# Kernel optimization log

Hardware: AMD Instinct MI355X
Metric: run time of the kernel (lower is better)

Reference implementation:

```python
import jax, jax.numpy as jnp
import numpy as np

B, S, D = 16, 1024, 768
H = 12
DH = D // H  # 64

def setup_inputs() -> dict:
    key = jax.random.key(0)
    ks = jax.random.split(key, 7)
    scale = 1.0 / np.sqrt(D)
    return {
        "hidden_states": jax.random.normal(ks[0], (B, S, D), dtype=jnp.float32),
        "Wq": jax.random.normal(ks[1], (D, D), dtype=jnp.float32) * scale,
        "bq": jnp.zeros((D,), dtype=jnp.float32),
        "Wk": jax.random.normal(ks[2], (D, D), dtype=jnp.float32) * scale,
        "bk": jnp.zeros((D,), dtype=jnp.float32),
        "Wv": jax.random.normal(ks[3], (D, D), dtype=jnp.float32) * scale,
        "bv": jnp.zeros((D,), dtype=jnp.float32),
    }

def reference(hidden_states, Wq, bq, Wk, bk, Wv, bv):
    # QKV projections: [B,S,D] -> [B,S,H,DH] -> [B,H,S,DH]
    def proj(W, b):
        y = hidden_states @ W.T + b
        return y.reshape(B, S, H, DH).transpose(0, 2, 1, 3)
    q = proj(Wq, bq)
    k = proj(Wk, bk)
    v = proj(Wv, bv)
    # attention scores [B,H,S,S], scaled by sqrt(d_head)
    scores = jnp.einsum('bhqd,bhkd->bhqk', q, k) / jnp.sqrt(jnp.float32(DH))
    probs = jax.nn.softmax(scores, axis=-1)
    # dropout prob = 0.0 (eval) -> identity
    ctx = jnp.einsum('bhqk,bhkd->bhqd', probs, v)
    ctx = ctx.transpose(0, 2, 1, 3).reshape(B, S, D)
    return ctx
```

## Files before the change

kernel.cpp:

```cpp
#include <hip/hip_runtime.h>
#include <hip/hip_bf16.h>

typedef __attribute__((ext_vector_type(8))) short short8;
typedef __attribute__((ext_vector_type(4))) float float4v;
typedef __attribute__((ext_vector_type(2))) unsigned int uint2v;

#define MFMA_BF16 __builtin_amdgcn_mfma_f32_16x16x32_bf16

__device__ __forceinline__ unsigned short f2b(float f) {
  union { float f; unsigned u; } v; v.f = f;
  unsigned r = v.u + 0x7FFFu + ((v.u >> 16) & 1u);
  return (unsigned short)(r >> 16);
}

__device__ __forceinline__ unsigned pk2(float x, float y) {
  float2 v; v.x = x; v.y = y;
  __hip_bfloat162 h = __float22bfloat162_rn(v);
  union { __hip_bfloat162 h; unsigned u; } c; c.h = h;
  return c.u;
}

__device__ __forceinline__ void gld16(const unsigned short* g, unsigned short* l) {
  __builtin_amdgcn_global_load_lds(
      (const __attribute__((address_space(1))) unsigned int*)g,
      (__attribute__((address_space(3))) unsigned int*)l, 16, 0, 0);
}

__device__ __forceinline__ int swa(int r, int k) {
  return (r << 6) + ((((k >> 3) ^ r ^ (r >> 3)) & 7) << 3) + (k & 7);
}

__global__ __launch_bounds__(256) void cast_all(
    const float* __restrict__ hs, const float* __restrict__ Wq,
    const float* __restrict__ Wk, const float* __restrict__ Wv,
    unsigned short* __restrict__ Xb, unsigned short* __restrict__ Wb) {
  const int blk = blockIdx.x;
  const float* src;
  unsigned short* dst;
  int i;
  if (blk < 12288) {
    i = blk * 256 + threadIdx.x;
    src = hs;
    dst = Xb;
  } else {
    const int x = blk - 12288;
    const int z = x / 576;
    i = (x - z * 576) * 256 + threadIdx.x;
    src = (z == 0) ? Wq : (z == 1 ? Wk : Wv);
    dst = Wb + (size_t)z * 589824;
  }
  float4 f = ((const float4*)src)[i];
  uint2 o;
  o.x = pk2(f.x, f.y);
  o.y = pk2(f.z, f.w);
  ((uint2*)dst)[i] = o;
}

__global__ __launch_bounds__(512) void qkv_gemm(
    const unsigned short* __restrict__ X, const unsigned short* __restrict__ Wall,
    const float* __restrict__ b0, const float* __restrict__ b1, const float* __restrict__ b2,
    unsigned short* __restrict__ O0, unsigned short* __restrict__ O1, unsigned short* __restrict__ OVT) {
  extern __shared__ __align__(16) unsigned short LDS[];

  const int g = blockIdx.x;
  const int orig = (g & 7) * 144 + (g >> 3);
  const int mblk = orig / 18;
  const int nblk = orig - mblk * 18;
  const int m0 = mblk * 256, n0p = nblk * 128;

  const int t = threadIdx.x, w = t >> 6, l = t & 63, qd = l >> 4, col = l & 15;
  const int wm64 = (w & 3) * 64, wn64 = (w >> 2) * 64;
  const int qd8 = qd * 8;

  const int cA0 = t, cA1 = 512 + t, cA2 = 1024 + t, cA3 = 1536 + t;
  const int rA0 = cA0 >> 3, rA1 = cA1 >> 3, rA2 = cA2 >> 3, rA3 = cA3 >> 3;
  const int pA0 = (cA0 ^ rA0 ^ (rA0 >> 3)) & 7, pA1 = (cA1 ^ rA1 ^ (rA1 >> 3)) & 7;
  const int pA2 = (cA2 ^ rA2 ^ (rA2 >> 3)) & 7, pA3 = (cA3 ^ rA3 ^ (rA3 >> 3)) & 7;
  const int cB0 = t, cB1 = 512 + t;
  const int rB0 = cB0 >> 3, rB1 = cB1 >> 3;
  const int pB0 = (cB0 ^ rB0 ^ (rB0 >> 3)) & 7, pB1 = (cB1 ^ rB1 ^ (rB1 >> 3)) & 7;

  const unsigned short* Xa0 = X + (size_t)(m0 + rA0) * 768 + pA0 * 8;
  const unsigned short* Xa1 = X + (size_t)(m0 + rA1) * 768 + pA1 * 8;
  const unsigned short* Xa2 = X + (size_t)(m0 + rA2) * 768 + pA2 * 8;
  const unsigned short* Xa3 = X + (size_t)(m0 + rA3) * 768 + pA3 * 8;
  const unsigned short* Wb0 = Wall + (size_t)(n0p + rB0) * 768 + pB0 * 8;
  const unsigned short* Wb1 = Wall + (size_t)(n0p + rB1) * 768 + pB1 * 8;
  const int dA0 = cA0 * 8, dA1 = cA1 * 8, dA2 = cA2 * 8, dA3 = cA3 * 8;
  const int dB0 = cB0 * 8, dB1 = cB1 * 8;

#define STAGE(kt, sb)                                         \
  do {                                                        \
    unsigned short* SA_ = LDS + (sb)*24576;                   \
    unsigned short* SB_ = SA_ + 16384;                        \
    const int kk_ = (kt)*64;                                  \
    gld16(Xa0 + kk_, SA_ + dA0);                              \
    gld16(Xa1 + kk_, SA_ + dA1);                              \
    gld16(Xa2 + kk_, SA_ + dA2);                              \
    gld16(Xa3 + kk_, SA_ + dA3);                              \
    gld16(Wb0 + kk_, SB_ + dB0);                              \
    gld16(Wb1 + kk_, SB_ + dB1);                              \
  } while (0)

  float4v acc[4][4];
#pragma unroll
  for (int i = 0; i < 4; ++i)
#pragma unroll
    for (int j = 0; j < 4; ++j) acc[i][j] = (float4v)0.0f;

#define COMPUTE(cur)                                                          \
  do {                                                                        \
    const unsigned short* Ar_ = LDS + (cur)*24576;                            \
    const unsigned short* Br_ = Ar_ + 16384;                                  \
    _Pragma("unroll") for (int ks = 0; ks < 2; ++ks) {                        \
      short8 af[4], bf[4];                                                    \
      _Pragma("unroll") for (int mi = 0; mi < 4; ++mi)                        \
          af[mi] = *(const short8*)&Ar_[swa(wm64 + mi * 16 + col,             \
                                            ks * 32 + qd8)];                  \
      _Pragma("unroll") for (int ni = 0; ni < 4; ++ni)                        \
          bf[ni] = *(const short8*)&Br_[swa(wn64 + ni * 16 + col,             \
                                            ks * 32 + qd8)];                  \
      __builtin_amdgcn_s_setprio(1);                                          \
      _Pragma("unroll") for (int mi = 0; mi < 4; ++mi)                        \
          _Pragma("unroll") for (int ni = 0; ni < 4; ++ni)                    \
          acc[mi][ni] = MFMA_BF16(af[mi], bf[ni], acc[mi][ni], 0, 0, 0);      \
      __builtin_amdgcn_s_setprio(0);                                          \
    }                                                                         \
  } while (0)

  STAGE(0, 0);
  STAGE(1, 1);
  asm volatile("s_waitcnt vmcnt(6)" ::: "memory");
  __builtin_amdgcn_s_barrier();
  __builtin_amdgcn_sched_barrier(0);

  int cur = 0;
#pragma unroll 1
  for (int kt = 0; kt < 10; ++kt) {
    const int sb = (cur == 0) ? 2 : cur - 1;
    STAGE(kt + 2, sb);
    COMPUTE(cur);
    asm volatile("s_waitcnt vmcnt(6)" ::: "memory");
    __builtin_amdgcn_s_barrier();
    __builtin_amdgcn_sched_barrier(0);
    cur = (cur == 2) ? 0 : cur + 1;
  }
  COMPUTE(cur);
  asm volatile("s_waitcnt vmcnt(0)" ::: "memory");
  __builtin_amdgcn_s_barrier();
  __builtin_amdgcn_sched_barrier(0);
  cur = (cur == 2) ? 0 : cur + 1;
  COMPUTE(cur);

  const int zz = n0p / 768;
  const int nbase = n0p - zz * 768;

  if (zz < 2) {
    unsigned short* O = (zz == 0) ? O0 : O1;
    const float* bias = (zz == 0) ? b0 : b1;
    const float osc = (zz == 0) ? 0.18033688f : 1.0f;
#pragma unroll
    for (int ni = 0; ni < 4; ++ni) {
      const int n = nbase + wn64 + ni * 16 + col;
      const float bb = bias[n];
#pragma unroll
      for (int mi = 0; mi < 4; ++mi)
#pragma unroll
        for (int r = 0; r < 4; ++r) {
          const int m = m0 + wm64 + mi * 16 + qd * 4 + r;
          O[(size_t)m * 768 + n] = f2b((acc[mi][ni][r] + bb) * osc);
        }
    }
  } else {
    __syncthreads();
    unsigned short* T = LDS;
#pragma unroll
    for (int ni = 0; ni < 4; ++ni) {
      const int nl = wn64 + ni * 16 + col;
      const float bb = b2[nbase + nl];
#pragma unroll
      for (int mi = 0; mi < 4; ++mi) {
        const int ml = wm64 + mi * 16 + qd * 4;
        const int mc = ml >> 3;
        ushort4 o;
        o.x = f2b(acc[mi][ni][0] + bb);
        o.y = f2b(acc[mi][ni][1] + bb);
        o.z = f2b(acc[mi][ni][2] + bb);
        o.w = f2b(acc[mi][ni][3] + bb);
        *(ushort4*)&T[(nl << 8) + (((mc ^ (nl & 31)) & 31) << 3) + (ml & 7)] = o;
      }
    }
    __syncthreads();
    const int nl2 = t >> 2;
    const int seg = t & 3;
    const int nglob = nbase + nl2;
    const int hh = nglob >> 6, dd = nglob & 63;
    const int bb2 = m0 >> 10;
    unsigned short* dstp =
        &OVT[(((size_t)bb2 * 12 + hh) * 64 + dd) * 1024 + (m0 & 1023) + seg * 64];
#pragma unroll
    for (int j = 0; j < 8; ++j) {
      const int mc = seg * 8 + j;
      uint4 vv = *(const uint4*)&T[(nl2 << 8) + (((mc ^ (nl2 & 31)) & 31) << 3)];
      *(uint4*)&dstp[j * 8] = vv;
    }
  }
#undef STAGE
#undef COMPUTE
}

__global__ __launch_bounds__(256) void attn(
    const unsigned short* __restrict__ Q, const unsigned short* __restrict__ K,
    const unsigned short* __restrict__ VT, float* __restrict__ O) {
  __shared__ __align__(16) unsigned short Ks0[4096];
  __shared__ __align__(16) unsigned short Ks1[4096];
  __shared__ __align__(16) unsigned short Vt0[4096];
  __shared__ __align__(16) unsigned short Vt1[4096];

  const int g = blockIdx.x;
  const int orig = (g & 7) * 192 + (g >> 3);
  const int qt = orig & 7;
  const int hb = orig >> 3;
  const int b = hb / 12;
  const int h = hb - b * 12;

  const int t = threadIdx.x, w = t >> 6, l = t & 63, qd = l >> 4, col = l & 15;
  const size_t bh = (size_t)b * 786432 + (size_t)h * 64;
  const unsigned short* Kb = K + bh;
  const unsigned short* VTb = VT + ((size_t)(b * 12 + h)) * 65536;

  short8 qf[2][2];
  {
    const unsigned short* Qg = Q + bh + (size_t)(qt * 128 + w * 32) * 768;
#pragma unroll
    for (int mi = 0; mi < 2; ++mi)
#pragma unroll
      for (int ks = 0; ks < 2; ++ks)
        qf[mi][ks] =
            *(const short8*)&Qg[(size_t)(mi * 16 + col) * 768 + ks * 32 + qd * 8];
  }

  const int c0 = t, c1 = 256 + t;
  const int r0 = c0 >> 3, cc0 = (c0 ^ r0 ^ (r0 >> 3)) & 7;
  const int r1 = c1 >> 3, cc1 = (c1 ^ r1 ^ (r1 >> 3)) & 7;

#define STAGE_K(ktile, dst)                                             \
  do {                                                                  \
    const unsigned short* Kg_ = Kb + (size_t)(ktile)*49152;             \
    gld16(&Kg_[(size_t)r0 * 768 + cc0 * 8], &dst[c0 * 8]);              \
    gld16(&Kg_[(size_t)r1 * 768 + cc1 * 8], &dst[c1 * 8]);              \
  } while (0)

#define STAGE_V(ktile, dst)                                             \
  do {                                                                  \
    const unsigned short* Vg_ = VTb + (ktile)*64;                       \
    gld16(&Vg_[(size_t)r0 * 1024 + cc0 * 8], &dst[c0 * 8]);             \
    gld16(&Vg_[(size_t)r1 * 1024 + cc1 * 8], &dst[c1 * 8]);             \
  } while (0)

  STAGE_K(0, Ks0);
  STAGE_V(0, Vt0);

  float4v acc[2][4];
  float4v accl[2];
#pragma unroll
  for (int mi = 0; mi < 2; ++mi) {
    accl[mi] = (float4v)0.0f;
#pragma unroll
    for (int dt = 0; dt < 4; ++dt) acc[mi][dt] = (float4v)0.0f;
  }

  short8 ones;
#pragma unroll
  for (int j = 0; j < 8; ++j) ones[j] = (short)0x3F80;

  __syncthreads();

#define ATTN_ITER(kt, KsR, VtR, KsW, VtW)                                 \
  do {                                                                    \
    if ((kt) < 15) {                                                      \
      STAGE_K((kt) + 1, KsW);                                             \
      STAGE_V((kt) + 1, VtW);                                             \
    }                                                                     \
    short8 kf[2][4];                                                      \
    _Pragma("unroll") for (int ks = 0; ks < 2; ++ks)                      \
        _Pragma("unroll") for (int ni = 0; ni < 4; ++ni)                  \
        kf[ks][ni] =                                                      \
        *(const short8*)&KsR[swa(ni * 16 + col, ks * 32 + qd * 8)];       \
    float4v sT[2][4];                                                     \
    _Pragma("unroll") for (int mi = 0; mi < 2; ++mi)                      \
        _Pragma("unroll") for (int ni = 0; ni < 4; ++ni)                  \
        sT[mi][ni] = (float4v)0.0f;                                       \
    __builtin_amdgcn_s_setprio(1);                                        \
    _Pragma("unroll") for (int ks = 0; ks < 2; ++ks)                      \
        _Pragma("unroll") for (int ni = 0; ni < 4; ++ni) {                \
      sT[0][ni] = MFMA_BF16(kf[ks][ni], qf[0][ks], sT[0][ni], 0, 0, 0);   \
      sT[1][ni] = MFMA_BF16(kf[ks][ni], qf[1][ks], sT[1][ni], 0, 0, 0);   \
    }                                                                     \
    __builtin_amdgcn_s_setprio(0);                                        \
    _Pragma("unroll") for (int s = 0; s < 2; ++s) {                       \
      short8 pf[2];                                                       \
      _Pragma("unroll") for (int mi = 0; mi < 2; ++mi) {                  \
        float4v sa = sT[mi][s * 2 + 0];                                   \
        float4v sb = sT[mi][s * 2 + 1];                                   \
        unsigned A0 = pk2(__builtin_amdgcn_exp2f(sa[0]),                  \
                          __builtin_amdgcn_exp2f(sa[1]));                 \
        unsigned A1 = pk2(__builtin_amdgcn_exp2f(sa[2]),                  \
                          __builtin_amdgcn_exp2f(sa[3]));                 \
        unsigned B0 = pk2(__builtin_amdgcn_exp2f(sb[0]),                  \
                          __builtin_amdgcn_exp2f(sb[1]));                 \
        unsigned B1 = pk2(__builtin_amdgcn_exp2f(sb[2]),                  \
                          __builtin_amdgcn_exp2f(sb[3]));                 \
        uint2v x0 = __builtin_amdgcn_permlane32_swap(A0, B0, false, false);   \
        uint2v x1 = __builtin_amdgcn_permlane32_swap(A1, B1, false, false);   \
        uint2v y02 = __builtin_amdgcn_permlane16_swap(x0[0], x0[1], false, false); \
        uint2v y13 = __builtin_amdgcn_permlane16_swap(x1[0], x1[1], false, false); \
        union { unsigned u[4]; short8 v; } pu;                            \
        pu.u[0] = y02[0]; pu.u[1] = y13[0];                               \
        pu.u[2] = y02[1]; pu.u[3] = y13[1];                               \
        pf[mi] = pu.v;                                                    \
      }                                                                   \
      const int kk = s * 32 + qd * 8;                                     \
      __builtin_amdgcn_s_setprio(1);                                      \
      _Pragma("unroll") for (int dt = 0; dt < 4; ++dt) {                  \
        short8 vf = *(const short8*)&VtR[swa(dt * 16 + col, kk)];         \
        acc[0][dt] = MFMA_BF16(vf, pf[0], acc[0][dt], 0, 0, 0);           \
        acc[1][dt] = MFMA_BF16(vf, pf[1], acc[1][dt], 0, 0, 0);           \
      }                                                                   \
      accl[0] = MFMA_BF16(ones, pf[0], accl[0], 0, 0, 0);                 \
      accl[1] = MFMA_BF16(ones, pf[1], accl[1], 0, 0, 0);                 \
      __builtin_amdgcn_s_setprio(0);                                      \
    }                                                                     \
    __syncthreads();                                                      \
  } while (0)

  for (int kt2 = 0; kt2 < 16; kt2 += 2) {
    ATTN_ITER(kt2, Ks0, Vt0, Ks1, Vt1);
    ATTN_ITER(kt2 + 1, Ks1, Vt1, Ks0, Vt0);
  }

  float* Og = O + (size_t)(b * 1024 + qt * 128) * 768 + h * 64;
#pragma unroll
  for (int mi = 0; mi < 2; ++mi) {
    const float rl = 1.0f / accl[mi][0];
    const int q = w * 32 + mi * 16 + col;
#pragma unroll
    for (int dt = 0; dt < 4; ++dt) {
      float4 o;
      o.x = acc[mi][dt][0] * rl;
      o.y = acc[mi][dt][1] * rl;
      o.z = acc[mi][dt][2] * rl;
      o.w = acc[mi][dt][3] * rl;
      *(float4*)&Og[(size_t)q * 768 + dt * 16 + qd * 4] = o;
    }
  }
#undef STAGE_K
#undef STAGE_V
#undef ATTN_ITER
}

extern "C" void kernel_launch(void* const* d_in, const int* in_sizes, int n_in,
                              void* d_out, int out_size, void* d_ws, size_t ws_size,
                              hipStream_t stream) {
  const float* hs = (const float*)d_in[0];
  const float* Wq = (const float*)d_in[1];
  const float* bq = (const float*)d_in[2];
  const float* Wk = (const float*)d_in[3];
  const float* bk = (const float*)d_in[4];
  const float* Wv = (const float*)d_in[5];
  const float* bv = (const float*)d_in[6];
  float* out = (float*)d_out;
  char* ws = (char*)d_ws;

  unsigned short* Xb = (unsigned short*)ws;
  unsigned short* Wb = (unsigned short*)(ws + 25165824);
  unsigned short* Qb = (unsigned short*)(ws + 28704768);
  unsigned short* Kb = (unsigned short*)(ws + 53870592);
  unsigned short* Vb = (unsigned short*)(ws + 79036416);

  static bool attr_set = false;
  if (!attr_set) {
    hipFuncSetAttribute((const void*)qkv_gemm,
                        hipFuncAttributeMaxDynamicSharedMemorySize, 147456);
    attr_set = true;
  }

  cast_all<<<14016, 256, 0, stream>>>(hs, Wq, Wk, Wv, Xb, Wb);

  qkv_gemm<<<dim3(1152), 512, 147456, stream>>>(Xb, Wb, bq, bk, bv, Qb, Kb, Vb);

  attn<<<dim3(1536), 256, 0, stream>>>(Qb, Kb, Vb, out);
}
```

Measured before the change: 258.6 us.

## Fuse fp32-to-bf16 cast into QKV GEMM loads, drop separate cast kernel

Removes the standalone cast kernel. The QKV GEMM now reads fp32 activations and weights from global memory into registers, converts them to bf16, and writes them to swizzled LDS. The pipeline changes from a 3-stage direct global-to-LDS async copy to a 2-stage register-staged double buffer with __syncthreads. This saves one kernel launch and the bf16 round trip through memory, but the GEMM now reads twice as many bytes per tile (fp32), and each weight is converted many times across blocks. It also loses the deeper async pipeline.

New measurement: 320.7 us. +24.0%, slower.

```diff
diff --git a/kernel.cpp b/kernel.cpp
--- a/kernel.cpp
+++ b/kernel.cpp
@@ -30,34 +30,9 @@
   return (r << 6) + ((((k >> 3) ^ r ^ (r >> 3)) & 7) << 3) + (k & 7);
 }
 
-__global__ __launch_bounds__(256) void cast_all(
-    const float* __restrict__ hs, const float* __restrict__ Wq,
-    const float* __restrict__ Wk, const float* __restrict__ Wv,
-    unsigned short* __restrict__ Xb, unsigned short* __restrict__ Wb) {
-  const int blk = blockIdx.x;
-  const float* src;
-  unsigned short* dst;
-  int i;
-  if (blk < 12288) {
-    i = blk * 256 + threadIdx.x;
-    src = hs;
-    dst = Xb;
-  } else {
-    const int x = blk - 12288;
-    const int z = x / 576;
-    i = (x - z * 576) * 256 + threadIdx.x;
-    src = (z == 0) ? Wq : (z == 1 ? Wk : Wv);
-    dst = Wb + (size_t)z * 589824;
-  }
-  float4 f = ((const float4*)src)[i];
-  uint2 o;
-  o.x = pk2(f.x, f.y);
-  o.y = pk2(f.z, f.w);
-  ((uint2*)dst)[i] = o;
-}
-
 __global__ __launch_bounds__(512) void qkv_gemm(
-    const unsigned short* __restrict__ X, const unsigned short* __restrict__ Wall,
+    const float* __restrict__ Xf, const float* __restrict__ Wqf,
+    const float* __restrict__ Wkf, const float* __restrict__ Wvf,
     const float* __restrict__ b0, const float* __restrict__ b1, const float* __restrict__ b2,
     unsigned short* __restrict__ O0, unsigned short* __restrict__ O1, unsigned short* __restrict__ OVT) {
   extern __shared__ __align__(16) unsigned short LDS[];
@@ -67,46 +42,68 @@
   const int mblk = orig / 18;
   const int nblk = orig - mblk * 18;
   const int m0 = mblk * 256, n0p = nblk * 128;
+  const int zz = n0p / 768;
+  const int nbase = n0p - zz * 768;
+  const float* Wf = (zz == 0) ? Wqf : (zz == 1 ? Wkf : Wvf);
 
   const int t = threadIdx.x, w = t >> 6, l = t & 63, qd = l >> 4, col = l & 15;
   const int wm64 = (w & 3) * 64, wn64 = (w >> 2) * 64;
   const int qd8 = qd * 8;
 
-  const int cA0 = t, cA1 = 512 + t, cA2 = 1024 + t, cA3 = 1536 + t;
-  const int rA0 = cA0 >> 3, rA1 = cA1 >> 3, rA2 = cA2 >> 3, rA3 = cA3 >> 3;
-  const int pA0 = (cA0 ^ rA0 ^ (rA0 >> 3)) & 7, pA1 = (cA1 ^ rA1 ^ (rA1 >> 3)) & 7;
-  const int pA2 = (cA2 ^ rA2 ^ (rA2 >> 3)) & 7, pA3 = (cA3 ^ rA3 ^ (rA3 >> 3)) & 7;
-  const int cB0 = t, cB1 = 512 + t;
-  const int rB0 = cB0 >> 3, rB1 = cB1 >> 3;
-  const int pB0 = (cB0 ^ rB0 ^ (rB0 >> 3)) & 7, pB1 = (cB1 ^ rB1 ^ (rB1 >> 3)) & 7;
-
-  const unsigned short* Xa0 = X + (size_t)(m0 + rA0) * 768 + pA0 * 8;
-  const unsigned short* Xa1 = X + (size_t)(m0 + rA1) * 768 + pA1 * 8;
-  const unsigned short* Xa2 = X + (size_t)(m0 + rA2) * 768 + pA2 * 8;
-  const unsigned short* Xa3 = X + (size_t)(m0 + rA3) * 768 + pA3 * 8;
-  const unsigned short* Wb0 = Wall + (size_t)(n0p + rB0) * 768 + pB0 * 8;
-  const unsigned short* Wb1 = Wall + (size_t)(n0p + rB1) * 768 + pB1 * 8;
-  const int dA0 = cA0 * 8, dA1 = cA1 * 8, dA2 = cA2 * 8, dA3 = cA3 * 8;
-  const int dB0 = cB0 * 8, dB1 = cB1 * 8;
-
-#define STAGE(kt, sb)                                         \
-  do {                                                        \
-    unsigned short* SA_ = LDS + (sb)*24576;                   \
-    unsigned short* SB_ = SA_ + 16384;                        \
-    const int kk_ = (kt)*64;                                  \
-    gld16(Xa0 + kk_, SA_ + dA0);                              \
-    gld16(Xa1 + kk_, SA_ + dA1);                              \
-    gld16(Xa2 + kk_, SA_ + dA2);                              \
-    gld16(Xa3 + kk_, SA_ + dA3);                              \
-    gld16(Wb0 + kk_, SB_ + dB0);                              \
-    gld16(Wb1 + kk_, SB_ + dB1);                              \
+  const int j = t & 7, tr = t >> 3;
+  const int rA0 = tr, rA1 = 64 + tr, rA2 = 128 + tr, rA3 = 192 + tr;
+  const int rB0 = tr, rB1 = 64 + tr;
+  const int dA0 = (rA0 << 6) + (((j ^ rA0 ^ (rA0 >> 3)) & 7) << 3);
+  const int dA1 = (rA1 << 6) + (((j ^ rA1 ^ (rA1 >> 3)) & 7) << 3);
+  const int dA2 = (rA2 << 6) + (((j ^ rA2 ^ (rA2 >> 3)) & 7) << 3);
+  const int dA3 = (rA3 << 6) + (((j ^ rA3 ^ (rA3 >> 3)) & 7) << 3);
+  const int dB0 = (rB0 << 6) + (((j ^ rB0 ^ (rB0 >> 3)) & 7) << 3);
+  const int dB1 = (rB1 << 6) + (((j ^ rB1 ^ (rB1 >> 3)) & 7) << 3);
+  const float* XA0 = Xf + (size_t)(m0 + rA0) * 768 + j * 8;
+  const float* XA1 = Xf + (size_t)(m0 + rA1) * 768 + j * 8;
+  const float* XA2 = Xf + (size_t)(m0 + rA2) * 768 + j * 8;
+  const float* XA3 = Xf + (size_t)(m0 + rA3) * 768 + j * 8;
+  const float* WB0 = Wf + (size_t)(nbase + rB0) * 768 + j * 8;
+  const float* WB1 = Wf + (size_t)(nbase + rB1) * 768 + j * 8;
+
+  float4 a0, a1, a2, a3, a4, a5, a6, a7, g0, g1, g2, g3;
+
+#define LOADR(kt)                                              \
+  do {                                                         \
+    const int kk_ = (kt)*64;                                   \
+    a0 = *(const float4*)(XA0 + kk_); a1 = *(const float4*)(XA0 + kk_ + 4); \
+    a2 = *(const float4*)(XA1 + kk_); a3 = *(const float4*)(XA1 + kk_ + 4); \
+    a4 = *(const float4*)(XA2 + kk_); a5 = *(const float4*)(XA2 + kk_ + 4); \
+    a6 = *(const float4*)(XA3 + kk_); a7 = *(const float4*)(XA3 + kk_ + 4); \
+    g0 = *(const float4*)(WB0 + kk_); g1 = *(const float4*)(WB0 + kk_ + 4); \
+    g2 = *(const float4*)(WB1 + kk_); g3 = *(const float4*)(WB1 + kk_ + 4); \
+  } while (0)
+
+#define CVW(base, dst, lo, hi)                                 \
+  do {                                                         \
+    uint4 pv_;                                                 \
+    pv_.x = pk2(lo.x, lo.y); pv_.y = pk2(lo.z, lo.w);          \
+    pv_.z = pk2(hi.x, hi.y); pv_.w = pk2(hi.z, hi.w);          \
+    *(uint4*)&base[dst] = pv_;                                 \
+  } while (0)
+
+#define WRITEALL(sb)                                           \
+  do {                                                         \
+    unsigned short* SA_ = LDS + (sb)*24576;                    \
+    unsigned short* SB_ = SA_ + 16384;                         \
+    CVW(SA_, dA0, a0, a1);                                     \
+    CVW(SA_, dA1, a2, a3);                                     \
+    CVW(SA_, dA2, a4, a5);                                     \
+    CVW(SA_, dA3, a6, a7);                                     \
+    CVW(SB_, dB0, g0, g1);                                     \
+    CVW(SB_, dB1, g2, g3);                                     \
   } while (0)
 
   float4v acc[4][4];
 #pragma unroll
   for (int i = 0; i < 4; ++i)
 #pragma unroll
-    for (int j = 0; j < 4; ++j) acc[i][j] = (float4v)0.0f;
+    for (int jj = 0; jj < 4; ++jj) acc[i][jj] = (float4v)0.0f;
 
 #define COMPUTE(cur)                                                          \
   do {                                                                        \
@@ -128,32 +125,21 @@
     }                                                                         \
   } while (0)
 
-  STAGE(0, 0);
-  STAGE(1, 1);
-  asm volatile("s_waitcnt vmcnt(6)" ::: "memory");
-  __builtin_amdgcn_s_barrier();
-  __builtin_amdgcn_sched_barrier(0);
+  LOADR(0);
+  WRITEALL(0);
+  __syncthreads();
 
   int cur = 0;
 #pragma unroll 1
-  for (int kt = 0; kt < 10; ++kt) {
-    const int sb = (cur == 0) ? 2 : cur - 1;
-    STAGE(kt + 2, sb);
+  for (int kt = 0; kt < 11; ++kt) {
+    LOADR(kt + 1);
+    __builtin_amdgcn_sched_barrier(0);
     COMPUTE(cur);
-    asm volatile("s_waitcnt vmcnt(6)" ::: "memory");
-    __builtin_amdgcn_s_barrier();
-    __builtin_amdgcn_sched_barrier(0);
-    cur = (cur == 2) ? 0 : cur + 1;
+    WRITEALL(cur ^ 1);
+    __syncthreads();
+    cur ^= 1;
   }
   COMPUTE(cur);
-  asm volatile("s_waitcnt vmcnt(0)" ::: "memory");
-  __builtin_amdgcn_s_barrier();
-  __builtin_amdgcn_sched_barrier(0);
-  cur = (cur == 2) ? 0 : cur + 1;
-  COMPUTE(cur);
-
-  const int zz = n0p / 768;
-  const int nbase = n0p - zz * 768;
 
   if (zz < 2) {
     unsigned short* O = (zz == 0) ? O0 : O1;
@@ -199,13 +185,15 @@
     unsigned short* dstp =
         &OVT[(((size_t)bb2 * 12 + hh) * 64 + dd) * 1024 + (m0 & 1023) + seg * 64];
 #pragma unroll
-    for (int j = 0; j < 8; ++j) {
-      const int mc = seg * 8 + j;
+    for (int jj = 0; jj < 8; ++jj) {
+      const int mc = seg * 8 + jj;
       uint4 vv = *(const uint4*)&T[(nl2 << 8) + (((mc ^ (nl2 & 31)) & 31) << 3)];
-      *(uint4*)&dstp[j * 8] = vv;
+      *(uint4*)&dstp[jj * 8] = vv;
     }
   }
-#undef STAGE
+#undef LOADR
+#undef CVW
+#undef WRITEALL
 #undef COMPUTE
 }
 
@@ -272,7 +260,7 @@
 
   short8 ones;
 #pragma unroll
-  for (int j = 0; j < 8; ++j) ones[j] = (short)0x3F80;
+  for (int jj = 0; jj < 8; ++jj) ones[jj] = (short)0x3F80;
 
   __syncthreads();
 
@@ -372,22 +360,19 @@
   float* out = (float*)d_out;
   char* ws = (char*)d_ws;
 
-  unsigned short* Xb = (unsigned short*)ws;
-  unsigned short* Wb = (unsigned short*)(ws + 25165824);
-  unsigned short* Qb = (unsigned short*)(ws + 28704768);
-  unsigned short* Kb = (unsigned short*)(ws + 53870592);
-  unsigned short* Vb = (unsigned short*)(ws + 79036416);
+  unsigned short* Qb = (unsigned short*)ws;
+  unsigned short* Kb = (unsigned short*)(ws + 25165824);
+  unsigned short* Vb = (unsigned short*)(ws + 50331648);
 
   static bool attr_set = false;
   if (!attr_set) {
     hipFuncSetAttribute((const void*)qkv_gemm,
-                        hipFuncAttributeMaxDynamicSharedMemorySize, 147456);
+                        hipFuncAttributeMaxDynamicSharedMemorySize, 98304);
     attr_set = true;
   }
 
-  cast_all<<<14016, 256, 0, stream>>>(hs, Wq, Wk, Wv, Xb, Wb);
-
-  qkv_gemm<<<dim3(1152), 512, 147456, stream>>>(Xb, Wb, bq, bk, bv, Qb, Kb, Vb);
+  qkv_gemm<<<dim3(1152), 512, 98304, stream>>>(hs, Wq, Wk, Wv, bq, bk, bv,
+                                               Qb, Kb, Vb);
 
   attn<<<dim3(1536), 256, 0, stream>>>(Qb, Kb, Vb, out);
 }
```

## Software-pipeline attention loop with triple-buffered K/V and QK one tile ahead

Applied to the files above, without the earlier changes.

Restructures the attention inner loop so the QK^T MFMAs for tile kt run in the same step as the exp/softmax and PV work for tile kt-1. K is prefetched two tiles ahead and V one tile ahead through a third LDS buffer. Full __syncthreads is replaced by explicit vmcnt waits plus raw barriers. The goal is to hide exp/permlane latency and global-to-LDS load latency behind matrix work. In exchange it uses more LDS (48KB instead of 32KB) and keeps two score sets live in registers, which may reduce occupancy.

New measurement: 253.8 us. About the same (-1.9%).

```diff
diff --git a/kernel.cpp b/kernel.cpp
--- a/kernel.cpp
+++ b/kernel.cpp
@@ -214,8 +214,10 @@
     const unsigned short* __restrict__ VT, float* __restrict__ O) {
   __shared__ __align__(16) unsigned short Ks0[4096];
   __shared__ __align__(16) unsigned short Ks1[4096];
+  __shared__ __align__(16) unsigned short Ks2[4096];
   __shared__ __align__(16) unsigned short Vt0[4096];
   __shared__ __align__(16) unsigned short Vt1[4096];
+  __shared__ __align__(16) unsigned short Vt2[4096];
 
   const int g = blockIdx.x;
   const int orig = (g & 7) * 192 + (g >> 3);
@@ -258,9 +260,6 @@
     gld16(&Vg_[(size_t)r1 * 1024 + cc1 * 8], &dst[c1 * 8]);             \
   } while (0)
 
-  STAGE_K(0, Ks0);
-  STAGE_V(0, Vt0);
-
   float4v acc[2][4];
   float4v accl[2];
 #pragma unroll
@@ -269,40 +268,39 @@
 #pragma unroll
     for (int dt = 0; dt < 4; ++dt) acc[mi][dt] = (float4v)0.0f;
   }
+  float4v sA[2][4], sB[2][4];
+  const float4v Zv = (float4v)0.0f;
 
   short8 ones;
 #pragma unroll
   for (int j = 0; j < 8; ++j) ones[j] = (short)0x3F80;
 
-  __syncthreads();
-
-#define ATTN_ITER(kt, KsR, VtR, KsW, VtW)                                 \
+#define QK_TILE(KsR, S)                                                   \
   do {                                                                    \
-    if ((kt) < 15) {                                                      \
-      STAGE_K((kt) + 1, KsW);                                             \
-      STAGE_V((kt) + 1, VtW);                                             \
-    }                                                                     \
     short8 kf[2][4];                                                      \
     _Pragma("unroll") for (int ks = 0; ks < 2; ++ks)                      \
         _Pragma("unroll") for (int ni = 0; ni < 4; ++ni)                  \
         kf[ks][ni] =                                                      \
         *(const short8*)&KsR[swa(ni * 16 + col, ks * 32 + qd * 8)];       \
-    float4v sT[2][4];                                                     \
-    _Pragma("unroll") for (int mi = 0; mi < 2; ++mi)                      \
-        _Pragma("unroll") for (int ni = 0; ni < 4; ++ni)                  \
-        sT[mi][ni] = (float4v)0.0f;                                       \
     __builtin_amdgcn_s_setprio(1);                                        \
-    _Pragma("unroll") for (int ks = 0; ks < 2; ++ks)                      \
-        _Pragma("unroll") for (int ni = 0; ni < 4; ++ni) {                \
-      sT[0][ni] = MFMA_BF16(kf[ks][ni], qf[0][ks], sT[0][ni], 0, 0, 0);   \
-      sT[1][ni] = MFMA_BF16(kf[ks][ni], qf[1][ks], sT[1][ni], 0, 0, 0);   \
+    _Pragma("unroll") for (int ni = 0; ni < 4; ++ni) {                    \
+      S[0][ni] = MFMA_BF16(kf[0][ni], qf[0][0], Zv, 0, 0, 0);             \
+      S[1][ni] = MFMA_BF16(kf[0][ni], qf[1][0], Zv, 0, 0, 0);             \
+    }                                                                     \
+    _Pragma("unroll") for (int ni = 0; ni < 4; ++ni) {                    \
+      S[0][ni] = MFMA_BF16(kf[1][ni], qf[0][1], S[0][ni], 0, 0, 0);       \
+      S[1][ni] = MFMA_BF16(kf[1][ni], qf[1][1], S[1][ni], 0, 0, 0);       \
     }                                                                     \
     __builtin_amdgcn_s_setprio(0);                                        \
+  } while (0)
+
+#define SMPV(S, VtR)                                                      \
+  do {                                                                    \
     _Pragma("unroll") for (int s = 0; s < 2; ++s) {                       \
       short8 pf[2];                                                       \
       _Pragma("unroll") for (int mi = 0; mi < 2; ++mi) {                  \
-        float4v sa = sT[mi][s * 2 + 0];                                   \
-        float4v sb = sT[mi][s * 2 + 1];                                   \
+        float4v sa = S[mi][s * 2 + 0];                                    \
+        float4v sb = S[mi][s * 2 + 1];                                    \
         unsigned A0 = pk2(__builtin_amdgcn_exp2f(sa[0]),                  \
                           __builtin_amdgcn_exp2f(sa[1]));                 \
         unsigned A1 = pk2(__builtin_amdgcn_exp2f(sa[2]),                  \
@@ -331,13 +329,54 @@
       accl[1] = MFMA_BF16(ones, pf[1], accl[1], 0, 0, 0);                 \
       __builtin_amdgcn_s_setprio(0);                                      \
     }                                                                     \
-    __syncthreads();                                                      \
-  } while (0)
-
-  for (int kt2 = 0; kt2 < 16; kt2 += 2) {
-    ATTN_ITER(kt2, Ks0, Vt0, Ks1, Vt1);
-    ATTN_ITER(kt2 + 1, Ks1, Vt1, Ks0, Vt0);
-  }
+  } while (0)
+
+#define W4 asm volatile("s_waitcnt vmcnt(4)" ::: "memory")
+#define W2 asm volatile("s_waitcnt vmcnt(2)" ::: "memory")
+#define W0 asm volatile("s_waitcnt vmcnt(0)" ::: "memory")
+#define BAR                                                               \
+  do {                                                                    \
+    __builtin_amdgcn_s_barrier();                                         \
+    __builtin_amdgcn_sched_barrier(0);                                    \
+  } while (0)
+
+#define PIPE(kt, KR, VR, KW, VW, Snew, Sold, WAIT)                        \
+  do {                                                                    \
+    if ((kt) + 2 < 16) STAGE_K((kt) + 2, KW);                             \
+    if ((kt) + 1 < 16) STAGE_V((kt) + 1, VW);                             \
+    QK_TILE(KR, Snew);                                                    \
+    SMPV(Sold, VR);                                                       \
+    WAIT;                                                                 \
+    BAR;                                                                  \
+  } while (0)
+
+  STAGE_K(0, Ks0);
+  STAGE_V(0, Vt0);
+  STAGE_K(1, Ks1);
+  STAGE_V(1, Vt1);
+  STAGE_K(2, Ks2);
+  W0;
+  BAR;
+  QK_TILE(Ks0, sA);
+  BAR;
+
+  PIPE(1,  Ks1, Vt0, Ks0, Vt2, sB, sA, W4);
+  PIPE(2,  Ks2, Vt1, Ks1, Vt0, sA, sB, W4);
+  PIPE(3,  Ks0, Vt2, Ks2, Vt1, sB, sA, W4);
+  PIPE(4,  Ks1, Vt0, Ks0, Vt2, sA, sB, W4);
+  PIPE(5,  Ks2, Vt1, Ks1, Vt0, sB, sA, W4);
+  PIPE(6,  Ks0, Vt2, Ks2, Vt1, sA, sB, W4);
+  PIPE(7,  Ks1, Vt0, Ks0, Vt2, sB, sA, W4);
+  PIPE(8,  Ks2, Vt1, Ks1, Vt0, sA, sB, W4);
+  PIPE(9,  Ks0, Vt2, Ks2, Vt1, sB, sA, W4);
+  PIPE(10, Ks1, Vt0, Ks0, Vt2, sA, sB, W4);
+  PIPE(11, Ks2, Vt1, Ks1, Vt0, sB, sA, W4);
+  PIPE(12, Ks0, Vt2, Ks2, Vt1, sA, sB, W4);
+  PIPE(13, Ks1, Vt0, Ks0, Vt2, sB, sA, W4);
+  PIPE(14, Ks2, Vt1, Ks0, Vt0, sA, sB, W0);
+  QK_TILE(Ks0, sB);
+  SMPV(sA, Vt2);
+  SMPV(sB, Vt0);
 
   float* Og = O + (size_t)(b * 1024 + qt * 128) * 768 + h * 64;
 #pragma unroll
@@ -356,7 +395,13 @@
   }
 #undef STAGE_K
 #undef STAGE_V
-#undef ATTN_ITER
+#undef QK_TILE
+#undef SMPV
+#undef PIPE
+#undef W4
+#undef W2
+#undef W0
+#undef BAR
 }
 
 extern "C" void kernel_launch(void* const* d_in, const int* in_sizes, int n_in,
```
